# Kernel optimization log

Measured on AMD Instinct MI355X. Metric: run time of the kernel, lower is better.

Reference implementation:

```python
import jax, jax.numpy as jnp
import numpy as np
from jax import lax

K = 3            # kernel size of both shift and adder convs
PAD = 1
EPS = 1e-5       # BatchNorm eps (torch default)
THRESHOLD = 0.005  # SEConv2d shift-weight zeroing threshold


def shift_quant(w, threshold=THRESHOLD):
    """SEConv2d weight: sign(w) * 2^round(log2|w|), zeroed below threshold, with STE."""
    aw = jnp.abs(w)
    q = jnp.sign(w) * jnp.exp2(jnp.round(jnp.log2(jnp.maximum(aw, 1e-10))))
    q = jnp.where(aw < threshold, 0.0, q)
    return w + lax.stop_gradient(q - w)  # straight-through estimator


def shift_conv(x, w, stride=1):
    """3x3 conv with power-of-two (bit-shift) weights."""
    wq = shift_quant(w)
    return lax.conv_general_dilated(
        x, wq, window_strides=(stride, stride), padding=[(PAD, PAD), (PAD, PAD)],
        dimension_numbers=("NCHW", "OIHW", "NCHW"))


def adder_conv(x, w):
    """AdderNet 3x3 conv, stride 1, pad 1: out = -sum |patch - weight| (L1 distance).
    Loops over output channels with lax.map to avoid the [N,Cout,Cin*K*K,L] blowup."""
    N, Cin, H, W = x.shape
    Cout = w.shape[0]
    # patches: [N, Cin*K*K, H, W], feature dim ordered (channel, kh, kw) -> matches w.reshape
    patches = lax.conv_general_dilated_patches(
        x, filter_shape=(K, K), window_strides=(1, 1), padding=[(PAD, PAD), (PAD, PAD)])
    Ck = patches.shape[1]
    p = patches.reshape(N, Ck, H * W)          # [N, Ck, L]
    wf = w.reshape(Cout, Ck)                   # [Cout, Ck]

    def per_channel(wc):                       # wc: [Ck]
        return -jnp.sum(jnp.abs(p - wc[None, :, None]), axis=1)  # [N, L]

    out = lax.map(per_channel, wf)             # [Cout, N, L]
    return out.transpose(1, 0, 2).reshape(N, Cout, H, W)


def batchnorm(x, gamma, beta):
    """BatchNorm2d in training mode (batch statistics over N,H,W)."""
    mean = jnp.mean(x, axis=(0, 2, 3), keepdims=True)
    var = jnp.var(x, axis=(0, 2, 3), keepdims=True)
    xn = (x - mean) * lax.rsqrt(var + EPS)
    return xn * gamma[None, :, None, None] + beta[None, :, None, None]


def setup_inputs() -> dict:
    key = jax.random.key(0)
    ks = jax.random.split(key, 5)
    N, C, H, W = 32, 128, 28, 28
    std = 1.0 / np.sqrt(C * K * K)
    x = jax.random.normal(ks[0], (N, C, H, W), dtype=jnp.float32)
    w_shift1 = jax.random.normal(ks[1], (C, C, K, K), dtype=jnp.float32) * std
    w_add1 = jax.random.normal(ks[2], (C, C, K, K), dtype=jnp.float32) * std
    w_shift2 = jax.random.normal(ks[3], (C, C, K, K), dtype=jnp.float32) * std
    w_add2 = jax.random.normal(ks[4], (C, C, K, K), dtype=jnp.float32) * std
    return {
        "x": x,
        "w_shift1": w_shift1, "w_add1": w_add1,
        "bn1_gamma": jnp.ones((C,), jnp.float32), "bn1_beta": jnp.zeros((C,), jnp.float32),
        "w_shift2": w_shift2, "w_add2": w_add2,
        "bn2_gamma": jnp.ones((C,), jnp.float32), "bn2_beta": jnp.zeros((C,), jnp.float32),
    }


def reference(x, w_shift1, w_add1, bn1_gamma, bn1_beta,
              w_shift2, w_add2, bn2_gamma, bn2_beta):
    residual = x
    out = adder_conv(shift_conv(x, w_shift1, stride=1), w_add1)   # conv1 = shift -> adder
    out = jax.nn.relu(batchnorm(out, bn1_gamma, bn1_beta))
    out = adder_conv(shift_conv(out, w_shift2, stride=1), w_add2)  # conv2
    out = batchnorm(out, bn2_gamma, bn2_beta)
    return jax.nn.relu(out + residual)
```

## Files before the change

kernel.cpp:

```cpp
#include <hip/hip_runtime.h>

#define PADH 30
#define PADW 32
#define CSTR (PADH*PADW)
#define NIMG 32
#define NCH  128
#define HW   28
#define PBUF ((size_t)NIMG*NCH*CSTR)
#define WREL (128*128*9)
#define WPACK (WREL/2)

#define QS16   4096.0f
#define QINV16 (-2.44140625e-04f)
#define QZERO16 0x80008000u

typedef __attribute__((ext_vector_type(8))) short bf16x8;
typedef __attribute__((ext_vector_type(4))) float f32x4;
typedef __attribute__((ext_vector_type(4))) unsigned u32x4;
typedef __attribute__((address_space(4))) const u32x4 cu32x4;

__device__ __forceinline__ unsigned short f2bf(float f) {
  unsigned u = __float_as_uint(f);
  return (unsigned short)((u + 0x7FFFu + ((u >> 16) & 1u)) >> 16);
}

__global__ __launch_bounds__(256) void prep_adder(
    const float* __restrict__ a1, const float* __restrict__ a2,
    unsigned* __restrict__ dst) {
  int gid = blockIdx.x * 256 + threadIdx.x;
  int t = gid / WPACK, r = gid % WPACK;
  const float* src = t ? a2 : a1;
  int co = r / 576;
  int rem = r % 576;
  int pair = rem / 9, tap = rem % 9;
  float v0 = src[co * 1152 + (2 * pair) * 9 + tap];
  float v1 = src[co * 1152 + (2 * pair + 1) * 9 + tap];
  unsigned q0 = __float2uint_rn((v0 + 8.0f) * QS16);
  unsigned q1 = __float2uint_rn((v1 + 8.0f) * QS16);
  int cog = co >> 2, j = co & 3;
  dst[(size_t)t * WPACK + (((cog * 64 + pair) * 9 + tap) << 2) + j] = q0 | (q1 << 16);
}

__global__ __launch_bounds__(256) void prep_shift(
    const float* __restrict__ s1, const float* __restrict__ s2,
    unsigned short* __restrict__ dst) {
  int gid = blockIdx.x * 256 + threadIdx.x;
  int t = gid / WREL, r = gid % WREL;
  float v = (t ? s2 : s1)[r];
  float aw = fabsf(v);
  if (aw < 0.005f) {
    v = 0.0f;
  } else {
    int e; float m = frexpf(aw, &e);
    int k = (m >= 0.70710678f) ? e : e - 1;
    v = ldexpf(copysignf(1.0f, v), k);
  }
  int co = r / 1152, rem = r % 1152;
  int ci = rem / 9, tap = rem % 9;
  int cog = co >> 4, cop = co & 15;
  dst[(size_t)t * WREL +
      ((((size_t)(cog * 9 + tap) * 4 + (ci >> 5)) * 16 + cop) * 32 + (ci & 31))] = f2bf(v);
}

__global__ __launch_bounds__(256) void pad_cl(
    const float* __restrict__ x, unsigned short* __restrict__ o) {
  __shared__ unsigned short tile[32 * 130];
  int n = blockIdx.x / PADH, yp = blockIdx.x % PADH;
  int tid = threadIdx.x;
  bool rowok = (yp >= 1 && yp <= HW);
#pragma unroll
  for (int it = 0; it < 16; ++it) {
    int idx = it * 256 + tid;
    int ci = idx >> 5, xp = idx & 31;
    float v = 0.0f;
    if (rowok && xp >= 1 && xp <= HW)
      v = x[(size_t)(n * NCH + ci) * (HW * HW) + (yp - 1) * HW + (xp - 1)];
    tile[xp * 130 + ci] = f2bf(v);
  }
  __syncthreads();
  unsigned int* ob = (unsigned int*)(o + (size_t)(n * PADH + yp) * 4096);
#pragma unroll
  for (int it = 0; it < 8; ++it) {
    int uidx = it * 256 + tid;
    int kc = uidx >> 9, xp = (uidx >> 4) & 31, cp = uidx & 15;
    int ci = kc * 32 + 2 * cp;
    ob[uidx] = *(const unsigned int*)&tile[xp * 130 + ci];
  }
}

__global__ __launch_bounds__(256) void bn_apply_relu_cl(
    const float* __restrict__ t, const float* __restrict__ sb,
    unsigned short* __restrict__ o) {
  __shared__ unsigned short tile[32 * 130];
  int n = blockIdx.x / PADH, yp = blockIdx.x % PADH;
  int tid = threadIdx.x;
  bool rowok = (yp >= 1 && yp <= HW);
#pragma unroll
  for (int it = 0; it < 16; ++it) {
    int idx = it * 256 + tid;
    int ci = idx >> 5, xp = idx & 31;
    float v = 0.0f;
    if (rowok && xp >= 1 && xp <= HW) {
      float tv = t[((size_t)(n * NCH + ci) * PADH + yp) * PADW + xp];
      v = fmaxf(fmaf(tv, sb[ci], sb[NCH + ci]), 0.0f);
    }
    tile[xp * 130 + ci] = f2bf(v);
  }
  __syncthreads();
  unsigned int* ob = (unsigned int*)(o + (size_t)(n * PADH + yp) * 4096);
#pragma unroll
  for (int it = 0; it < 8; ++it) {
    int uidx = it * 256 + tid;
    int kc = uidx >> 9, xp = (uidx >> 4) & 31, cp = uidx & 15;
    int ci = kc * 32 + 2 * cp;
    ob[uidx] = *(const unsigned int*)&tile[xp * 130 + ci];
  }
}

__global__ __launch_bounds__(256) void zero_halo(unsigned* __restrict__ b) {
  int gid = blockIdx.x * 256 + threadIdx.x;
  int nc = gid / 120, i = gid % 120;
  unsigned* p = b + (size_t)nc * CSTR;
  if (i < 64) {
    int row = (i < 32) ? 0 : (PADH - 1);
    p[row * PADW + (i & 31)] = QZERO16;
  } else {
    int i2 = i - 64;
    int row = 1 + (i2 >> 1);
    int col = (i2 & 1) ? (HW + 1) : 0;
    p[row * PADW + col] = QZERO16;
  }
}

__global__ __launch_bounds__(512) void shift_mfma(
    const unsigned short* __restrict__ in, const unsigned short* __restrict__ wq,
    unsigned* __restrict__ out) {
  __shared__ uint4 btile4[2048];
  char* btile = (char*)btile4;
  int bid = blockIdx.x;
  int vb = (bid & 7) * 196 + (bid >> 3);
  int pxt = vb % 49;
  int n = vb / 49;
  int cot = threadIdx.x >> 6;
  int lane = threadIdx.x & 63;
  int t = threadIdx.x;

  int px0 = pxt * 16;
  int y0 = px0 / HW;
#pragma unroll
  for (int it = 0; it < 4; ++it) {
    int rp = y0 + it; if (rp > 29) rp = 29;
    const uint4* src = (const uint4*)(in + (size_t)(n * PADH + rp) * 4096) + t;
    *(uint4*)(btile + it * 8192 + t * 16) = *src;
  }
  __syncthreads();

  int px = px0 + (lane & 15);
  int y = px / HW, x = px % HW;
  int iro = y - y0;
  int colb = (x + 1) * 64 + (lane >> 4) * 16;
  const unsigned short* wbase =
      wq + (size_t)cot * 18432 + (lane & 15) * 32 + (lane >> 4) * 8;

  f32x4 acc = {0.f, 0.f, 0.f, 0.f};
#pragma unroll
  for (int tap = 0; tap < 9; ++tap) {
    const int ky = tap / 3 - 1, kx = tap % 3 - 1;
    const char* lb = btile + (iro + ky + 1) * 8192 + colb + kx * 64;
    const unsigned short* wb = wbase + tap * 2048;
#pragma unroll
    for (int kc = 0; kc < 4; ++kc) {
      bf16x8 a = *(const bf16x8*)(wb + kc * 512);
      bf16x8 b = *(const bf16x8*)(lb + kc * 2048);
      acc = __builtin_amdgcn_mfma_f32_16x16x32_bf16(a, b, acc, 0, 0, 0);
    }
  }
  int coa = cot * 16 + (lane >> 4) * 4;
  unsigned q[4];
#pragma unroll
  for (int r = 0; r < 4; ++r) {
    float v = fminf(fmaxf(acc[r], -7.9f), 7.9f);
    q[r] = __float2uint_rn((v + 8.0f) * QS16);
  }
  int cp = coa >> 1;
  unsigned* ob = out + ((size_t)(n * 64 + cp) * PADH + (y + 1)) * PADW + (x + 1);
  ob[0] = q[0] | (q[1] << 16);
  ob[CSTR] = q[2] | (q[3] << 16);
}

__device__ __forceinline__ void sad16_op(unsigned& acc, unsigned vin, unsigned w) {
  asm("v_sad_u16 %0, %1, %2, %0" : "+v"(acc) : "v"(vin), "s"(w));
}

__device__ __forceinline__ void load_rows_u(const unsigned* __restrict__ p,
                                            unsigned r[3][4]) {
#pragma unroll
  for (int ky = 0; ky < 3; ++ky) {
    uint2 a = *(const uint2*)(p + ky * PADW);
    uint2 b = *(const uint2*)(p + ky * PADW + 2);
    r[ky][0] = a.x; r[ky][1] = a.y; r[ky][2] = b.x; r[ky][3] = b.y;
  }
}

__device__ __forceinline__ void adder_ci_reg(const unsigned r[3][4],
                                             const u32x4 w[9],
                                             unsigned acc[4][2]) {
#pragma unroll
  for (int ky = 0; ky < 3; ++ky)
#pragma unroll
    for (int kx = 0; kx < 3; ++kx) {
      u32x4 wA = w[ky * 3 + kx];
#pragma unroll
      for (int p = 0; p < 2; ++p) {
        unsigned v = r[ky][kx + p];
        sad16_op(acc[0][p], v, wA.x);
        sad16_op(acc[1][p], v, wA.y);
        sad16_op(acc[2][p], v, wA.z);
        sad16_op(acc[3][p], v, wA.w);
      }
    }
}

__global__ __launch_bounds__(256) void adder_conv(
    const unsigned* __restrict__ in, const unsigned* __restrict__ wr,
    float* __restrict__ out, double* __restrict__ ps) {
  int bid = blockIdx.x;
  int v = (bid & 7) * 196 + (bid >> 3);
  int cog = v & 31;
  int chunk = v >> 5;
  int tid = threadIdx.x;

  int wi = chunk * 256 + tid;
  int xh = wi % 14;
  int r2 = wi / 14;
  int y = r2 % 28;
  int n = r2 / 28;
  int x0 = xh << 1;
  const unsigned* ib = in + (size_t)n * 64 * CSTR + y * PADW + x0;
  cu32x4* w4 = (cu32x4*)(wr + (size_t)cog * 2304);

  unsigned acc[4][2];
#pragma unroll
  for (int j = 0; j < 4; ++j) { acc[j][0] = 0u; acc[j][1] = 0u; }

  u32x4 cw[9], nw[9];
#pragma unroll
  for (int t = 0; t < 9; ++t) cw[t] = w4[t];
  unsigned ra[3][4], rb[3][4];
  load_rows_u(ib, ra);

  for (int cp = 0; cp < 64; cp += 2) {
#pragma unroll
    for (int t = 0; t < 9; ++t) nw[t] = w4[(cp + 1) * 9 + t];
    load_rows_u(ib + CSTR, rb);
    adder_ci_reg(ra, cw, acc);
    if (cp + 2 < 64) {
#pragma unroll
      for (int t = 0; t < 9; ++t) cw[t] = w4[(cp + 2) * 9 + t];
      load_rows_u(ib + 2 * CSTR, ra);
    }
    adder_ci_reg(rb, nw, acc);
    ib += 2 * CSTR;
  }

  float vout[4][2];
#pragma unroll
  for (int j = 0; j < 4; ++j) {
    vout[j][0] = (float)acc[j][0] * QINV16;
    vout[j][1] = (float)acc[j][1] * QINV16;
  }
  float* ob = out + ((size_t)(n * NCH + (cog << 2)) * PADH + (y + 1)) * PADW + (x0 + 1);
#pragma unroll
  for (int j = 0; j < 4; ++j) {
    ob[j * CSTR + 0] = vout[j][0];
    ob[j * CSTR + 1] = vout[j][1];
  }

  __shared__ double wred[4][8];
  int wv = tid >> 6, ln = tid & 63;
#pragma unroll
  for (int j = 0; j < 4; ++j) {
    double s  = (double)vout[j][0] + (double)vout[j][1];
    double s2 = (double)vout[j][0] * vout[j][0] + (double)vout[j][1] * vout[j][1];
#pragma unroll
    for (int off = 32; off > 0; off >>= 1) {
      s  += __shfl_down(s, off, 64);
      s2 += __shfl_down(s2, off, 64);
    }
    if (ln == 0) { wred[wv][j * 2] = s; wred[wv][j * 2 + 1] = s2; }
  }
  __syncthreads();
  if (tid == 0) {
#pragma unroll
    for (int j = 0; j < 4; ++j) {
      double S = 0.0, S2 = 0.0;
#pragma unroll
      for (int w8 = 0; w8 < 4; ++w8) { S += wred[w8][j * 2]; S2 += wred[w8][j * 2 + 1]; }
      ps[((size_t)(cog * 49 + chunk) * 4 + j) * 2]     = S;
      ps[((size_t)(cog * 49 + chunk) * 4 + j) * 2 + 1] = S2;
    }
  }
}

__global__ __launch_bounds__(128) void bn_finalize(
    const double* __restrict__ ps, const float* __restrict__ gamma,
    const float* __restrict__ beta, float* __restrict__ sb) {
  int c = threadIdx.x;
  int cog = c >> 2, j = c & 3;
  double s = 0.0, s2 = 0.0;
  for (int ch = 0; ch < 49; ++ch) {
    s  += ps[((size_t)(cog * 49 + ch) * 4 + j) * 2];
    s2 += ps[((size_t)(cog * 49 + ch) * 4 + j) * 2 + 1];
  }
  double cnt = (double)(NIMG * HW * HW);
  double mean = s / cnt;
  double var = s2 / cnt - mean * mean;
  double rstd = 1.0 / sqrt(var + 1e-5);
  double g = (double)gamma[c];
  sb[c] = (float)(g * rstd);
  sb[NCH + c] = (float)((double)beta[c] - mean * g * rstd);
}

__global__ __launch_bounds__(256) void final_kernel(
    const float* __restrict__ t5, const float* __restrict__ sb,
    const float* __restrict__ x, float* __restrict__ out) {
  int idx = blockIdx.x * 256 + threadIdx.x;
  int f = idx * 4;
  int n = f / (NCH * HW * HW);
  int c = (f / (HW * HW)) % NCH;
  int o = f % (HW * HW);
  int y = o / HW, xc = o % HW;
  const float* tp = t5 + ((size_t)(n * NCH + c) * PADH + y + 1) * PADW + xc + 1;
  float sc = sb[c], bi = sb[NCH + c];
  float4 xv = *(const float4*)(x + f);
  float4 ov;
  ov.x = fmaxf(fmaf(tp[0], sc, bi) + xv.x, 0.0f);
  ov.y = fmaxf(fmaf(tp[1], sc, bi) + xv.y, 0.0f);
  ov.z = fmaxf(fmaf(tp[2], sc, bi) + xv.z, 0.0f);
  ov.w = fmaxf(fmaf(tp[3], sc, bi) + xv.w, 0.0f);
  *(float4*)(out + f) = ov;
}

extern "C" void kernel_launch(void* const* d_in, const int* in_sizes, int n_in,
                              void* d_out, int out_size, void* d_ws, size_t ws_size,
                              hipStream_t stream) {
  const float* x   = (const float*)d_in[0];
  const float* ws1 = (const float*)d_in[1];
  const float* wa1 = (const float*)d_in[2];
  const float* g1  = (const float*)d_in[3];
  const float* b1  = (const float*)d_in[4];
  const float* ws2 = (const float*)d_in[5];
  const float* wa2 = (const float*)d_in[6];
  const float* g2  = (const float*)d_in[7];
  const float* b2  = (const float*)d_in[8];
  float* out = (float*)d_out;

  float* w = (float*)d_ws;
  unsigned* P1 = (unsigned*)w;
  float* P2 = w + PBUF;
  unsigned short* CL0 = (unsigned short*)(w + 2 * PBUF);
  unsigned short* CL1 = CL0 + PBUF;
  float* WAf = w + 3 * PBUF;
  unsigned* WA = (unsigned*)WAf;
  unsigned short* WS = (unsigned short*)(WAf + 2 * (size_t)WREL);
  float* SB1 = WAf + 3 * (size_t)WREL;
  float* SB2 = SB1 + 256;
  double* PS = (double*)(SB2 + 256);

  hipLaunchKernelGGL(prep_adder,      dim3(576),  dim3(256), 0, stream, wa1, wa2, WA);
  hipLaunchKernelGGL(prep_shift,      dim3(1152), dim3(256), 0, stream, ws1, ws2, WS);
  hipLaunchKernelGGL(pad_cl,          dim3(960),  dim3(256), 0, stream, x, CL0);
  hipLaunchKernelGGL(zero_halo,       dim3(960),  dim3(256), 0, stream, P1);
  hipLaunchKernelGGL(shift_mfma,      dim3(1568), dim3(512), 0, stream, CL0, WS, P1);
  hipLaunchKernelGGL(adder_conv,      dim3(1568), dim3(256), 0, stream, P1, WA, P2, PS);
  hipLaunchKernelGGL(bn_finalize,     dim3(1),    dim3(128), 0, stream, PS, g1, b1, SB1);
  hipLaunchKernelGGL(bn_apply_relu_cl,dim3(960),  dim3(256), 0, stream, P2, SB1, CL1);
  hipLaunchKernelGGL(shift_mfma,      dim3(1568), dim3(512), 0, stream, CL1, WS + WREL, P1);
  hipLaunchKernelGGL(adder_conv,      dim3(1568), dim3(256), 0, stream, P1, WA + WPACK, P2, PS);
  hipLaunchKernelGGL(bn_finalize,     dim3(1),    dim3(128), 0, stream, PS, g2, b2, SB2);
  hipLaunchKernelGGL(final_kernel,    dim3(3136), dim3(256), 0, stream, P2, SB2, x, out);
}
```

Baseline: 250.5 us.

## Stage adder-conv input rows in LDS with channel-major packed layout

Changes the packed input layout so each channel-pair plane stores all images contiguously, letting a block's rows for one channel pair be read as one contiguous span. The adder kernel now cooperatively loads that span into a double-buffered shared-memory tile and reads the 3x3 neighborhoods from LDS instead of redundant global loads. This removes overlapping global reads across threads, at the cost of two block barriers per channel pair and extra shared-memory traffic.

```diff
diff --git a/kernel.cpp b/kernel.cpp
--- a/kernel.cpp
+++ b/kernel.cpp
@@ -7,6 +7,7 @@
 #define NCH  128
 #define HW   28
 #define PBUF ((size_t)NIMG*NCH*CSTR)
+#define NPSTR (NIMG*CSTR)
 #define WREL (128*128*9)
 #define WPACK (WREL/2)
 
@@ -183,21 +184,21 @@
     q[r] = __float2uint_rn((v + 8.0f) * QS16);
   }
   int cp = coa >> 1;
-  unsigned* ob = out + ((size_t)(n * 64 + cp) * PADH + (y + 1)) * PADW + (x + 1);
+  unsigned* ob = out + ((size_t)cp * NIMG + n) * CSTR + (y + 1) * PADW + (x + 1);
   ob[0] = q[0] | (q[1] << 16);
-  ob[CSTR] = q[2] | (q[3] << 16);
+  ob[NPSTR] = q[2] | (q[3] << 16);
 }
 
 __device__ __forceinline__ void sad16_op(unsigned& acc, unsigned vin, unsigned w) {
   asm("v_sad_u16 %0, %1, %2, %0" : "+v"(acc) : "v"(vin), "s"(w));
 }
 
-__device__ __forceinline__ void load_rows_u(const unsigned* __restrict__ p,
-                                            unsigned r[3][4]) {
+__device__ __forceinline__ void load_rows_lds(const unsigned* __restrict__ L,
+                                              int base, unsigned r[3][4]) {
 #pragma unroll
   for (int ky = 0; ky < 3; ++ky) {
-    uint2 a = *(const uint2*)(p + ky * PADW);
-    uint2 b = *(const uint2*)(p + ky * PADW + 2);
+    uint2 a = *(const uint2*)&L[base + ky * 32];
+    uint2 b = *(const uint2*)&L[base + ky * 32 + 2];
     r[ky][0] = a.x; r[ky][1] = a.y; r[ky][2] = b.x; r[ky][3] = b.y;
   }
 }
@@ -224,6 +225,7 @@
 __global__ __launch_bounds__(256) void adder_conv(
     const unsigned* __restrict__ in, const unsigned* __restrict__ wr,
     float* __restrict__ out, double* __restrict__ ps) {
+  __shared__ unsigned lbuf[2][768];
   int bid = blockIdx.x;
   int v = (bid & 7) * 196 + (bid >> 3);
   int cog = v & 31;
@@ -236,7 +238,11 @@
   int y = r2 % 28;
   int n = r2 / 28;
   int x0 = xh << 1;
-  const unsigned* ib = in + (size_t)n * 64 * CSTR + y * PADW + x0;
+
+  int r2lo = (chunk * 256) / 14;
+  int g0 = (r2lo / 28) * 30 + (r2lo % 28);
+  int lbase = (n * 30 + y - g0) * 32 + x0;
+
   cu32x4* w4 = (cu32x4*)(wr + (size_t)cog * 2304);
 
   unsigned acc[4][2];
@@ -246,21 +252,36 @@
   u32x4 cw[9], nw[9];
 #pragma unroll
   for (int t = 0; t < 9; ++t) cw[t] = w4[t];
-  unsigned ra[3][4], rb[3][4];
-  load_rows_u(ib, ra);
-
+
+  {
+    const unsigned* s = in + (size_t)g0 * PADW;
+#pragma unroll
+    for (int k = 0; k < 3; ++k) lbuf[0][k * 256 + tid] = s[k * 256 + tid];
+  }
+  __syncthreads();
+
+  unsigned ra[3][4];
   for (int cp = 0; cp < 64; cp += 2) {
+    {
+      const unsigned* s = in + (size_t)(cp + 1) * NPSTR + (size_t)g0 * PADW;
+#pragma unroll
+      for (int k = 0; k < 3; ++k) lbuf[1][k * 256 + tid] = s[k * 256 + tid];
+    }
 #pragma unroll
     for (int t = 0; t < 9; ++t) nw[t] = w4[(cp + 1) * 9 + t];
-    load_rows_u(ib + CSTR, rb);
+    load_rows_lds(lbuf[0], lbase, ra);
     adder_ci_reg(ra, cw, acc);
+    __syncthreads();
     if (cp + 2 < 64) {
+      const unsigned* s = in + (size_t)(cp + 2) * NPSTR + (size_t)g0 * PADW;
+#pragma unroll
+      for (int k = 0; k < 3; ++k) lbuf[0][k * 256 + tid] = s[k * 256 + tid];
 #pragma unroll
       for (int t = 0; t < 9; ++t) cw[t] = w4[(cp + 2) * 9 + t];
-      load_rows_u(ib + 2 * CSTR, ra);
-    }
-    adder_ci_reg(rb, nw, acc);
-    ib += 2 * CSTR;
+    }
+    load_rows_lds(lbuf[1], lbase, ra);
+    adder_ci_reg(ra, nw, acc);
+    __syncthreads();
   }
 
   float vout[4][2];
```

Result: slower. 279.2 us (+11.5%).
